# Optimization experiments

Measured on AMD Instinct MI355X. Metric: run time of the kernel, lower is better.

Reference implementation:

```python
import jax, jax.numpy as jnp
import numpy as np

EMBED_DIM = 1024
NUM_HEADS = 16
HEAD_DIM = EMBED_DIM // NUM_HEADS


def setup_inputs() -> dict:
    key = jax.random.key(0)
    ks = jax.random.split(key, 7)
    B, S, D = 8, 1024, EMBED_DIM
    scale = 1.0 / np.sqrt(D)
    x = jax.random.normal(ks[0], (B, S, D), dtype=jnp.float32)
    Wq = jax.random.normal(ks[1], (D, D), dtype=jnp.float32) * scale
    Wk = jax.random.normal(ks[2], (D, D), dtype=jnp.float32) * scale
    Wv = jax.random.normal(ks[3], (D, D), dtype=jnp.float32) * scale
    bq = jax.random.normal(ks[4], (D,), dtype=jnp.float32) * 0.01
    bk = jax.random.normal(ks[5], (D,), dtype=jnp.float32) * 0.01
    bv = jax.random.normal(ks[6], (D,), dtype=jnp.float32) * 0.01
    return {"x": x, "Wq": Wq, "Wk": Wk, "Wv": Wv, "bq": bq, "bk": bk, "bv": bv}


def reference(x, Wq, Wk, Wv, bq, bk, bv):
    B, S, D = x.shape
    H, Hd = NUM_HEADS, HEAD_DIM
    # torch nn.Linear: y = x @ W.T + b
    q = (x @ Wq.T + bq).reshape(B, S, H, Hd).transpose(0, 2, 1, 3)  # [B,H,S,Hd]
    k = (x @ Wk.T + bk).reshape(B, S, H, Hd).transpose(0, 2, 1, 3)
    v = (x @ Wv.T + bv).reshape(B, S, H, Hd).transpose(0, 2, 1, 3)
    scale = Hd ** -0.5
    scores = jnp.einsum('bhqd,bhkd->bhqk', q, k) * scale  # [B,H,S,S]
    attn = jax.nn.softmax(scores, axis=-1)
    # dropout_rate = 0.0 -> identity; out_proj is never applied in the source forward
    ctx = jnp.einsum('bhqk,bhkd->bhqd', attn, v)  # [B,H,S,Hd]
    return ctx.transpose(0, 2, 1, 3).reshape(B, S, D)
```

## Files before the change

### kernel.cpp

```cpp
#include <hip/hip_runtime.h>
#include <hip/hip_bf16.h>
#include <cstdint>
#include <cstddef>


typedef __attribute__((ext_vector_type(8))) short bf16x8;
typedef __attribute__((ext_vector_type(8))) unsigned short u16x8;
typedef __attribute__((ext_vector_type(4))) float f32x4;
typedef __attribute__((ext_vector_type(16))) float f32x16;
typedef __attribute__((ext_vector_type(4))) unsigned int u32x4;

typedef const __attribute__((address_space(1))) void* gptr_t;
typedef __attribute__((address_space(3))) void* lptr_t;

#define LOG2E 1.44269504088896340736f

__device__ __forceinline__ unsigned short f2bf(float f) {
  unsigned int u = __float_as_uint(f);
  u += 0x7fffu + ((u >> 16) & 1u);
  return (unsigned short)(u >> 16);
}

__device__ __forceinline__ unsigned int pack_bf16x2(float lo, float hi) {
  const __hip_bfloat162 h = __float22bfloat162_rn(float2{lo, hi});
  unsigned int u;
  __builtin_memcpy(&u, &h, 4);
  return u;
}

__device__ __forceinline__ float vmax16(const f32x16& v) {
  float a = fmaxf(fmaxf(v[0], v[1]), v[2]);
  float b = fmaxf(fmaxf(v[3], v[4]), v[5]);
  float c = fmaxf(fmaxf(v[6], v[7]), v[8]);
  float d = fmaxf(fmaxf(v[9], v[10]), v[11]);
  float e = fmaxf(fmaxf(v[12], v[13]), v[14]);
  float f = fmaxf(fmaxf(a, b), v[15]);
  float h = fmaxf(fmaxf(c, d), e);
  return fmaxf(f, h);
}

__global__ void cvt_f32_bf16(const float* __restrict__ src,
                             unsigned short* __restrict__ dst, int n4) {
  int i = blockIdx.x * blockDim.x + threadIdx.x;
  if (i >= n4) return;
  float4 v = reinterpret_cast<const float4*>(src)[i];
  ushort4 o;
  o.x = f2bf(v.x); o.y = f2bf(v.y); o.z = f2bf(v.z); o.w = f2bf(v.w);
  reinterpret_cast<ushort4*>(dst)[i] = o;
}

__global__ void cvt_w3(const float* __restrict__ wq, const float* __restrict__ wk,
                       const float* __restrict__ wv, unsigned short* __restrict__ dst) {
  const int b = blockIdx.x;
  const int sel = b >> 10;
  const float* src = (sel == 0) ? wq : (sel == 1) ? wk : wv;
  const int i = (b & 1023) * 256 + threadIdx.x;
  float4 v = reinterpret_cast<const float4*>(src)[i];
  ushort4 o;
  o.x = f2bf(v.x); o.y = f2bf(v.y); o.z = f2bf(v.z); o.w = f2bf(v.w);
  reinterpret_cast<ushort4*>(dst + (size_t)sel * 1048576)[i] = o;
}

__global__ __launch_bounds__(256) void qkv_gemm(
    const unsigned short* __restrict__ Xb, const unsigned short* __restrict__ Wb,
    const float* __restrict__ bq, const float* __restrict__ bk,
    const float* __restrict__ bv,
    unsigned short* __restrict__ Qo, unsigned short* __restrict__ Ko,
    unsigned short* __restrict__ Vo) {
  __shared__ unsigned short As[128 * 32];
  __shared__ unsigned short Bs[128 * 32];

  const int tid = threadIdx.x;
  const int lane = tid & 63;
  const int w = tid >> 6;
  const int wr = w >> 1, wc = w & 1;
  const int bm = blockIdx.x & 63;
  const int bn = blockIdx.x >> 6;

  const f32x4 vzero = {0.f, 0.f, 0.f, 0.f};
  f32x4 acc[4][4];
#pragma unroll
  for (int m = 0; m < 4; ++m)
#pragma unroll
    for (int n = 0; n < 4; ++n) acc[m][n] = vzero;

  const int c0 = w * 2, c1 = w * 2 + 1;
  const int srow0 = c0 * 16 + (lane >> 2);
  const int srow1 = c1 * 16 + (lane >> 2);
  const int scol = (lane & 3) * 8;
  const unsigned short* gA0 = Xb + (size_t)(bm * 128 + srow0) * 1024 + scol;
  const unsigned short* gA1 = Xb + (size_t)(bm * 128 + srow1) * 1024 + scol;
  const unsigned short* gB0 = Wb + (size_t)(bn * 128 + srow0) * 1024 + scol;
  const unsigned short* gB1 = Wb + (size_t)(bn * 128 + srow1) * 1024 + scol;
  char* lA0 = (char*)As + c0 * 1024;
  char* lA1 = (char*)As + c1 * 1024;
  char* lB0 = (char*)Bs + c0 * 1024;
  char* lB1 = (char*)Bs + c1 * 1024;

  const int aoff = (wr * 64 + (lane & 15)) * 64 + (lane >> 4) * 16;
  const int boff = (wc * 64 + (lane & 15)) * 64 + (lane >> 4) * 16;

  for (int kt = 0; kt < 32; ++kt) {
    const int k0 = kt * 32;
    __builtin_amdgcn_global_load_lds((gptr_t)(gA0 + k0), (lptr_t)lA0, 16, 0, 0);
    __builtin_amdgcn_global_load_lds((gptr_t)(gA1 + k0), (lptr_t)lA1, 16, 0, 0);
    __builtin_amdgcn_global_load_lds((gptr_t)(gB0 + k0), (lptr_t)lB0, 16, 0, 0);
    __builtin_amdgcn_global_load_lds((gptr_t)(gB1 + k0), (lptr_t)lB1, 16, 0, 0);
    __syncthreads();

    bf16x8 a[4], b[4];
#pragma unroll
    for (int m = 0; m < 4; ++m)
      a[m] = *reinterpret_cast<const bf16x8*>((const char*)As + aoff + m * 16 * 64);
#pragma unroll
    for (int n = 0; n < 4; ++n)
      b[n] = *reinterpret_cast<const bf16x8*>((const char*)Bs + boff + n * 16 * 64);
#pragma unroll
    for (int m = 0; m < 4; ++m)
#pragma unroll
      for (int n = 0; n < 4; ++n)
        acc[m][n] = __builtin_amdgcn_mfma_f32_16x16x32_bf16(a[m], b[n], acc[m][n], 0, 0, 0);
    __syncthreads();
  }

  const int t = bn >> 3;
  const float* bias = (t == 0) ? bq : (t == 1) ? bk : bv;
  unsigned short* dst = (t == 0) ? Qo : (t == 1) ? Ko : Vo;
  const float sc = (t == 0) ? 0.125f : 1.0f;
#pragma unroll
  for (int n = 0; n < 4; ++n) {
    const int gn = bn * 128 + wc * 64 + n * 16 + (lane & 15);
    const int d = gn & 1023;
    const int h = d >> 6, hd = d & 63;
    const float bias_v = bias[d];
#pragma unroll
    for (int m = 0; m < 4; ++m) {
      const int gm0 = bm * 128 + wr * 64 + m * 16 + ((lane >> 4) << 2);
      const int bb = gm0 >> 10;
      const int s0 = gm0 & 1023;
#pragma unroll
      for (int r = 0; r < 4; ++r) {
        dst[(((size_t)bb * 16 + h) * 1024 + (size_t)(s0 + r)) * 64 + hd] =
            f2bf((acc[m][n][r] + bias_v) * sc);
      }
    }
  }
}

__global__ __launch_bounds__(256) void transpose_v(
    const unsigned short* __restrict__ Vn, unsigned short* __restrict__ Vt) {
  __shared__ __align__(16) unsigned short T[64][72];
  const int tid = threadIdx.x;
  const int head = blockIdx.x & 127;
  const int st = blockIdx.x >> 7;
  const unsigned short* src = Vn + (size_t)head * 65536 + (size_t)st * 64 * 64;
  unsigned short* dst = Vt + (size_t)head * 65536 + (size_t)st * 64;
#pragma unroll
  for (int i = 0; i < 2; ++i) {
    const int idx = tid + i * 256;
    const int r = idx >> 3, ch = idx & 7;
    u16x8 v = *reinterpret_cast<const u16x8*>(src + r * 64 + ch * 8);
#pragma unroll
    for (int j = 0; j < 8; ++j)
      T[ch * 8 + j][r ^ (ch << 3)] = (unsigned short)v[j];
  }
  __syncthreads();
#pragma unroll
  for (int i = 0; i < 2; ++i) {
    const int idx = tid + i * 256;
    const int d = idx >> 3, ch = idx & 7;
    u16x8 v = *reinterpret_cast<const u16x8*>(&T[d][(ch ^ (d >> 3)) << 3]);
    *reinterpret_cast<u16x8*>(dst + (size_t)d * 1024 + ch * 8) = v;
  }
}

__global__ __launch_bounds__(256, 3) void attn32(
    const unsigned short* __restrict__ Q, const unsigned short* __restrict__ K,
    const unsigned short* __restrict__ Vt, float* __restrict__ out) {
  __shared__ __align__(16) char smem[3][16384];

  const int tid = threadIdx.x;
  const int lane = tid & 63;
  const int ln31 = lane & 31;
  const int g = lane >> 5;
  const int w = tid >> 6;
  const int head = blockIdx.x & 127;
  const int qt = blockIdx.x >> 7;

  const unsigned short* Qh = Q + (size_t)head * 65536;
  const unsigned short* Kh = K + (size_t)head * 65536;
  const unsigned short* Vh = Vt + (size_t)head * 65536;

  const int qrow = qt * 128 + w * 32 + ln31;
  bf16x8 qf[4];
#pragma unroll
  for (int dc = 0; dc < 4; ++dc)
    qf[dc] = *reinterpret_cast<const bf16x8*>(Qh + (size_t)qrow * 64 + dc * 16 + g * 8);
  asm volatile("s_waitcnt vmcnt(0)" ::: "memory");

  const int lbA = w * 1024 + lane * 16;
  const int lbB = lbA + 4096;
  const int rA = lbA >> 7, rB = lbB >> 7;
  const int cA = ((((lbA >> 4) & 7) ^ (rA & 7)) << 3);
  const int cB = ((((lbB >> 4) & 7) ^ (rB & 7)) << 3);
  const unsigned short* gK0 = Kh + rA * 64 + cA;
  const unsigned short* gK1 = Kh + rB * 64 + cB;
  const unsigned short* gV0 = Vh + rA * 1024 + cA;
  const unsigned short* gV1 = Vh + rB * 1024 + cB;

#pragma unroll
  for (int pt = 0; pt < 2; ++pt) {
    char* b0 = smem[pt] + w * 1024;
    const int k1 = pt * 4096, k2 = pt * 64;
    __builtin_amdgcn_global_load_lds((gptr_t)(gK0 + k1), (lptr_t)b0, 16, 0, 0);
    __builtin_amdgcn_global_load_lds((gptr_t)(gK1 + k1), (lptr_t)(b0 + 4096), 16, 0, 0);
    __builtin_amdgcn_global_load_lds((gptr_t)(gV0 + k2), (lptr_t)(b0 + 8192), 16, 0, 0);
    __builtin_amdgcn_global_load_lds((gptr_t)(gV1 + k2), (lptr_t)(b0 + 12288), 16, 0, 0);
  }

  float m_ = -3e38f, l_ = 0.f;
  f32x16 acc0, acc1;
#pragma unroll
  for (int i = 0; i < 16; ++i) { acc0[i] = 0.f; acc1[i] = 0.f; }

  const int swz = (ln31 & 7) << 4;
  const int rowb0 = ln31 * 128;
  int boff[4];
#pragma unroll
  for (int dc = 0; dc < 4; ++dc) boff[dc] = ((((dc << 1) | g) << 4) ^ swz);

  for (int kt = 0; kt < 16; ++kt) {
    if (kt < 15) {
      asm volatile("s_waitcnt vmcnt(4)" ::: "memory");
    } else {
      asm volatile("s_waitcnt vmcnt(0)" ::: "memory");
    }
    __builtin_amdgcn_s_barrier();
    __builtin_amdgcn_sched_barrier(0);

    if (kt < 14) {
      char* nb = smem[(kt + 2) % 3] + w * 1024;
      const int k1 = (kt + 2) * 4096, k2 = (kt + 2) * 64;
      __builtin_amdgcn_global_load_lds((gptr_t)(gK0 + k1), (lptr_t)nb, 16, 0, 0);
      __builtin_amdgcn_global_load_lds((gptr_t)(gK1 + k1), (lptr_t)(nb + 4096), 16, 0, 0);
      __builtin_amdgcn_global_load_lds((gptr_t)(gV0 + k2), (lptr_t)(nb + 8192), 16, 0, 0);
      __builtin_amdgcn_global_load_lds((gptr_t)(gV1 + k2), (lptr_t)(nb + 12288), 16, 0, 0);
    }

    const char* Kb_ = smem[kt % 3] + rowb0;
    const char* Vb_ = Kb_ + 8192;

    f32x16 s0, s1;
#pragma unroll
    for (int i = 0; i < 16; ++i) { s0[i] = 0.f; s1[i] = 0.f; }
    __builtin_amdgcn_s_setprio(1);
#pragma unroll
    for (int dc = 0; dc < 4; ++dc) {
      bf16x8 kf0 = *reinterpret_cast<const bf16x8*>(Kb_ + boff[dc]);
      bf16x8 kf1 = *reinterpret_cast<const bf16x8*>(Kb_ + 4096 + boff[dc]);
      s0 = __builtin_amdgcn_mfma_f32_32x32x16_bf16(kf0, qf[dc], s0, 0, 0, 0);
      s1 = __builtin_amdgcn_mfma_f32_32x32x16_bf16(kf1, qf[dc], s1, 0, 0, 0);
    }
    __builtin_amdgcn_s_setprio(0);

    float tm = fmaxf(vmax16(s0), vmax16(s1));
    tm = fmaxf(tm, __shfl_xor(tm, 32));
    if (__any(tm > m_ + 5.0f)) {
      const float mn = fmaxf(m_, tm);
      const float al = exp2f((m_ - mn) * LOG2E);
      m_ = mn;
      l_ *= al;
#pragma unroll
      for (int i = 0; i < 16; ++i) { acc0[i] *= al; acc1[i] *= al; }
    }
    const float mnl = m_ * LOG2E;
    float ts = 0.f;

    unsigned int c_[8][2];
#pragma unroll
    for (int b = 0; b < 4; ++b) {
      const float p0 = exp2f(fmaf(s0[4 * b + 0], LOG2E, -mnl));
      const float p1 = exp2f(fmaf(s0[4 * b + 1], LOG2E, -mnl));
      const float p2 = exp2f(fmaf(s0[4 * b + 2], LOG2E, -mnl));
      const float p3 = exp2f(fmaf(s0[4 * b + 3], LOG2E, -mnl));
      ts += (p0 + p1) + (p2 + p3);
      c_[b][0] = pack_bf16x2(p0, p1);
      c_[b][1] = pack_bf16x2(p2, p3);
    }
#pragma unroll
    for (int b = 4; b < 8; ++b) {
      const float p0 = exp2f(fmaf(s1[4 * (b - 4) + 0], LOG2E, -mnl));
      const float p1 = exp2f(fmaf(s1[4 * (b - 4) + 1], LOG2E, -mnl));
      const float p2 = exp2f(fmaf(s1[4 * (b - 4) + 2], LOG2E, -mnl));
      const float p3 = exp2f(fmaf(s1[4 * (b - 4) + 3], LOG2E, -mnl));
      ts += (p0 + p1) + (p2 + p3);
      c_[b][0] = pack_bf16x2(p0, p1);
      c_[b][1] = pack_bf16x2(p2, p3);
    }
    ts += __shfl_xor(ts, 32);
    l_ += ts;

    __builtin_amdgcn_s_setprio(1);
#pragma unroll
    for (int t = 0; t < 4; ++t) {
      u32x4 pv;
#pragma unroll
      for (int i = 0; i < 2; ++i) {
        const unsigned int A = c_[2 * t][i], Bv = c_[2 * t + 1][i];
        const unsigned int y =
            (unsigned int)__shfl_xor((int)((g == 0) ? Bv : A), 32);
        pv[i]     = (g == 0) ? A : y;
        pv[i + 2] = (g == 0) ? y : Bv;
      }
      const bf16x8 pfv = __builtin_bit_cast(bf16x8, pv);
      bf16x8 vf0 = *reinterpret_cast<const bf16x8*>(Vb_ + boff[t]);
      bf16x8 vf1 = *reinterpret_cast<const bf16x8*>(Vb_ + 4096 + boff[t]);
      acc0 = __builtin_amdgcn_mfma_f32_32x32x16_bf16(vf0, pfv, acc0, 0, 0, 0);
      acc1 = __builtin_amdgcn_mfma_f32_32x32x16_bf16(vf1, pfv, acc1, 0, 0, 0);
    }
    __builtin_amdgcn_s_setprio(0);
  }

  const float invl = 1.0f / l_;
  const int bb = head >> 4, hh = head & 15;
  float* orow = out + ((size_t)bb * 1024 + qrow) * 1024 + hh * 64;
#pragma unroll
  for (int rq = 0; rq < 4; ++rq) {
    const int d0 = rq * 8 + g * 4;
    float4 v0, v1;
    v0.x = acc0[rq * 4 + 0] * invl; v0.y = acc0[rq * 4 + 1] * invl;
    v0.z = acc0[rq * 4 + 2] * invl; v0.w = acc0[rq * 4 + 3] * invl;
    v1.x = acc1[rq * 4 + 0] * invl; v1.y = acc1[rq * 4 + 1] * invl;
    v1.z = acc1[rq * 4 + 2] * invl; v1.w = acc1[rq * 4 + 3] * invl;
    *reinterpret_cast<float4*>(orow + d0) = v0;
    *reinterpret_cast<float4*>(orow + 32 + d0) = v1;
  }
}

extern "C" void kernel_launch(void* const* d_in, const int* in_sizes, int n_in,
                              void* d_out, int out_size, void* d_ws, size_t ws_size,
                              hipStream_t stream) {
  const float* x  = (const float*)d_in[0];
  const float* Wq = (const float*)d_in[1];
  const float* Wk = (const float*)d_in[2];
  const float* Wv = (const float*)d_in[3];
  const float* bq = (const float*)d_in[4];
  const float* bk = (const float*)d_in[5];
  const float* bv = (const float*)d_in[6];
  float* out = (float*)d_out;

  char* ws = (char*)d_ws;
  unsigned short* Xb = (unsigned short*)(ws);
  unsigned short* Wb = (unsigned short*)(ws + (size_t)16 * 1024 * 1024);
  unsigned short* Qb = (unsigned short*)(ws + (size_t)22 * 1024 * 1024);
  unsigned short* Kb = Qb + (size_t)8 * 1024 * 1024;
  unsigned short* Vb = Kb + (size_t)8 * 1024 * 1024;
  unsigned short* Vt = Xb;

  cvt_f32_bf16<<<8192, 256, 0, stream>>>(x, Xb, 2097152);
  cvt_w3<<<3072, 256, 0, stream>>>(Wq, Wk, Wv, Wb);

  qkv_gemm<<<1536, 256, 0, stream>>>(Xb, Wb, bq, bk, bv, Qb, Kb, Vb);

  transpose_v<<<2048, 256, 0, stream>>>(Vb, Vt);

  attn32<<<1024, 256, 0, stream>>>(Qb, Kb, Vt, out);
}
```

Baseline: 155.3 us.

## Use 512-thread attention blocks and permlane32_swap for half-wave exchanges

Doubles the attention block to 8 waves covering 256 query rows, so each wave issues only one K and one V global-to-LDS load per tile. The shared K/V tile is reused across twice as many queries, which halves per-tile load traffic per block. Cross-half-wave max, sum and P-fragment exchanges now use the permlane32_swap builtin instead of ds_bpermute-based shuffles. The risks are fewer blocks (512) for the GPU's CUs, heavier per-barrier synchronisation across 8 waves, and register pressure under the new launch bounds.

```diff
diff --git a/kernel.cpp b/kernel.cpp
--- a/kernel.cpp
+++ b/kernel.cpp
@@ -9,6 +9,7 @@
 typedef __attribute__((ext_vector_type(4))) float f32x4;
 typedef __attribute__((ext_vector_type(16))) float f32x16;
 typedef __attribute__((ext_vector_type(4))) unsigned int u32x4;
+typedef __attribute__((ext_vector_type(2))) unsigned int u32x2;
 
 typedef const __attribute__((address_space(1))) void* gptr_t;
 typedef __attribute__((address_space(3))) void* lptr_t;
@@ -174,7 +175,7 @@
   }
 }
 
-__global__ __launch_bounds__(256, 3) void attn32(
+__global__ __launch_bounds__(512, 4) void attn32(
     const unsigned short* __restrict__ Q, const unsigned short* __restrict__ K,
     const unsigned short* __restrict__ Vt, float* __restrict__ out) {
   __shared__ __align__(16) char smem[3][16384];
@@ -191,31 +192,24 @@
   const unsigned short* Kh = K + (size_t)head * 65536;
   const unsigned short* Vh = Vt + (size_t)head * 65536;
 
-  const int qrow = qt * 128 + w * 32 + ln31;
+  const int qrow = qt * 256 + w * 32 + ln31;
   bf16x8 qf[4];
 #pragma unroll
   for (int dc = 0; dc < 4; ++dc)
     qf[dc] = *reinterpret_cast<const bf16x8*>(Qh + (size_t)qrow * 64 + dc * 16 + g * 8);
   asm volatile("s_waitcnt vmcnt(0)" ::: "memory");
 
-  const int lbA = w * 1024 + lane * 16;
-  const int lbB = lbA + 4096;
-  const int rA = lbA >> 7, rB = lbB >> 7;
-  const int cA = ((((lbA >> 4) & 7) ^ (rA & 7)) << 3);
-  const int cB = ((((lbB >> 4) & 7) ^ (rB & 7)) << 3);
-  const unsigned short* gK0 = Kh + rA * 64 + cA;
-  const unsigned short* gK1 = Kh + rB * 64 + cB;
-  const unsigned short* gV0 = Vh + rA * 1024 + cA;
-  const unsigned short* gV1 = Vh + rB * 1024 + cB;
+  const int lb = w * 1024 + lane * 16;
+  const int r = lb >> 7;
+  const int c = ((((lb >> 4) & 7) ^ (r & 7)) << 3);
+  const unsigned short* gK = Kh + r * 64 + c;
+  const unsigned short* gV = Vh + r * 1024 + c;
 
 #pragma unroll
   for (int pt = 0; pt < 2; ++pt) {
     char* b0 = smem[pt] + w * 1024;
-    const int k1 = pt * 4096, k2 = pt * 64;
-    __builtin_amdgcn_global_load_lds((gptr_t)(gK0 + k1), (lptr_t)b0, 16, 0, 0);
-    __builtin_amdgcn_global_load_lds((gptr_t)(gK1 + k1), (lptr_t)(b0 + 4096), 16, 0, 0);
-    __builtin_amdgcn_global_load_lds((gptr_t)(gV0 + k2), (lptr_t)(b0 + 8192), 16, 0, 0);
-    __builtin_amdgcn_global_load_lds((gptr_t)(gV1 + k2), (lptr_t)(b0 + 12288), 16, 0, 0);
+    __builtin_amdgcn_global_load_lds((gptr_t)(gK + pt * 4096), (lptr_t)b0, 16, 0, 0);
+    __builtin_amdgcn_global_load_lds((gptr_t)(gV + pt * 64), (lptr_t)(b0 + 8192), 16, 0, 0);
   }
 
   float m_ = -3e38f, l_ = 0.f;
@@ -231,7 +225,7 @@
 
   for (int kt = 0; kt < 16; ++kt) {
     if (kt < 15) {
-      asm volatile("s_waitcnt vmcnt(4)" ::: "memory");
+      asm volatile("s_waitcnt vmcnt(2)" ::: "memory");
     } else {
       asm volatile("s_waitcnt vmcnt(0)" ::: "memory");
     }
@@ -240,11 +234,8 @@
 
     if (kt < 14) {
       char* nb = smem[(kt + 2) % 3] + w * 1024;
-      const int k1 = (kt + 2) * 4096, k2 = (kt + 2) * 64;
-      __builtin_amdgcn_global_load_lds((gptr_t)(gK0 + k1), (lptr_t)nb, 16, 0, 0);
-      __builtin_amdgcn_global_load_lds((gptr_t)(gK1 + k1), (lptr_t)(nb + 4096), 16, 0, 0);
-      __builtin_amdgcn_global_load_lds((gptr_t)(gV0 + k2), (lptr_t)(nb + 8192), 16, 0, 0);
-      __builtin_amdgcn_global_load_lds((gptr_t)(gV1 + k2), (lptr_t)(nb + 12288), 16, 0, 0);
+      __builtin_amdgcn_global_load_lds((gptr_t)(gK + (kt + 2) * 4096), (lptr_t)nb, 16, 0, 0);
+      __builtin_amdgcn_global_load_lds((gptr_t)(gV + (kt + 2) * 64), (lptr_t)(nb + 8192), 16, 0, 0);
     }
 
     const char* Kb_ = smem[kt % 3] + rowb0;
@@ -264,7 +255,11 @@
     __builtin_amdgcn_s_setprio(0);
 
     float tm = fmaxf(vmax16(s0), vmax16(s1));
-    tm = fmaxf(tm, __shfl_xor(tm, 32));
+    {
+      u32x2 rm = __builtin_amdgcn_permlane32_swap(
+          __float_as_uint(tm), __float_as_uint(tm), false, false);
+      tm = fmaxf(__uint_as_float(rm[0]), __uint_as_float(rm[1]));
+    }
     if (__any(tm > m_ + 5.0f)) {
       const float mn = fmaxf(m_, tm);
       const float al = exp2f((m_ - mn) * LOG2E);
@@ -297,7 +292,11 @@
       c_[b][0] = pack_bf16x2(p0, p1);
       c_[b][1] = pack_bf16x2(p2, p3);
     }
-    ts += __shfl_xor(ts, 32);
+    {
+      u32x2 rs = __builtin_amdgcn_permlane32_swap(
+          __float_as_uint(ts), __float_as_uint(ts), false, false);
+      ts = __uint_as_float(rs[0]) + __uint_as_float(rs[1]);
+    }
     l_ += ts;
 
     __builtin_amdgcn_s_setprio(1);
@@ -306,11 +305,10 @@
       u32x4 pv;
 #pragma unroll
       for (int i = 0; i < 2; ++i) {
-        const unsigned int A = c_[2 * t][i], Bv = c_[2 * t + 1][i];
-        const unsigned int y =
-            (unsigned int)__shfl_xor((int)((g == 0) ? Bv : A), 32);
-        pv[i]     = (g == 0) ? A : y;
-        pv[i + 2] = (g == 0) ? y : Bv;
+        u32x2 rr = __builtin_amdgcn_permlane32_swap(
+            c_[2 * t][i], c_[2 * t + 1][i], false, false);
+        pv[i] = rr[0];
+        pv[i + 2] = rr[1];
       }
       const bf16x8 pfv = __builtin_bit_cast(bf16x8, pv);
       bf16x8 vf0 = *reinterpret_cast<const bf16x8*>(Vb_ + boff[t]);
@@ -364,5 +362,5 @@
 
   transpose_v<<<2048, 256, 0, stream>>>(Vb, Vt);
 
-  attn32<<<1024, 256, 0, stream>>>(Qb, Kb, Vt, out);
-}
+  attn32<<<512, 512, 0, stream>>>(Qb, Kb, Vt, out);
+}
```

Result: faster. 148.1 us (-4.6%).
